# Performance work log

Measured on AMD Instinct MI355X. Metric: run time of the kernel, lower is better.

## Reference

```python
import jax, jax.numpy as jnp
import numpy as np
import math

B, CK, CV, O, T, H, W = 2, 64, 512, 2, 16, 30, 54


def setup_inputs() -> dict:
    key = jax.random.key(0)
    k1, k2, k3, k4, k5 = jax.random.split(key, 5)
    return {
        'query_key': jax.random.normal(k1, (B, CK, H, W), jnp.float32),
        'query_selection': jax.random.uniform(k2, (B, CK, H, W), jnp.float32),
        'memory_key': jax.random.normal(k3, (B, CK, T, H, W), jnp.float32),
        'memory_shrinkage': jax.random.uniform(k4, (B, 1, T, H, W), jnp.float32),
        'memory_value': jax.random.normal(k5, (B, O, CV, T, H, W), jnp.float32),
    }


def reference(query_key, query_selection, memory_key, memory_shrinkage, memory_value):
    b, ck, h, w = query_key.shape
    t = memory_key.shape[2]
    n = t * h * w          # memory bank size
    hw = h * w             # query size
    o, cv = memory_value.shape[1], memory_value.shape[2]

    mk = memory_key.reshape(b, ck, n)             # B CK N
    ms = memory_shrinkage.reshape(b, 1, n)        # B 1 N
    qk = query_key.reshape(b, ck, hw)             # B CK HW
    qe = query_selection.reshape(b, ck, hw)       # B CK HW

    # negative squared L2 distance, selection-weighted per channel:
    # -sum_c qe_c * (mk_c - qk_c)^2 = -a_sq + 2ab - b_sq
    a_sq = jnp.einsum('bcn,bcq->bnq', mk * mk, qe)          # B N HW
    two_ab = 2.0 * jnp.einsum('bcn,bcq->bnq', mk, qk * qe)  # B N HW
    b_sq = jnp.sum(qe * qk * qk, axis=1, keepdims=True)     # B 1 HW
    similarity = (-a_sq + two_ab - b_sq)
    # shrinkage scaling + 1/sqrt(CK)
    similarity = similarity * ms.reshape(b, n, 1) * (1.0 / math.sqrt(ck))

    # softmax over the memory axis N
    affinity = jax.nn.softmax(similarity, axis=1)           # B N HW

    # weighted readout
    mv = memory_value.reshape(b, o * cv, n)                 # B (O*CV) N
    mem = jnp.einsum('bvn,bnq->bvq', mv, affinity)          # B (O*CV) HW
    return mem.reshape(b, o, cv, h, w)
```

## Files before the change

### kernel.cpp

```cpp
#include <hip/hip_runtime.h>
#include <stdint.h>

#define NTOT 25920
#define OCV  1024
#define HW   1620
#define QPAD 1632
#define NBLK 810
#define KSP  8

#define MV2_STRIDE ((size_t)8 * NBLK * 4096)
#define MKP_STRIDE ((size_t)NTOT * 128)
#define QP_STRIDE  ((size_t)1664 * 128)
#define BSQ_STRIDE ((size_t)1664)
#define P_STRIDE   ((size_t)NBLK * QPAD * 32)
#define PO_STRIDE  ((size_t)KSP * OCV * QPAD)
#define LP_STRIDE  ((size_t)405 * QPAD)
#define LQ_STRIDE  ((size_t)QPAD)

typedef _Float16 f16x8 __attribute__((ext_vector_type(8)));
typedef _Float16 f16x4 __attribute__((ext_vector_type(4)));
typedef float f32x4 __attribute__((ext_vector_type(4)));

__device__ __forceinline__ void gload_lds16(const void* g, void* l) {
  __builtin_amdgcn_global_load_lds(
      (const __attribute__((address_space(1))) uint32_t*)g,
      (__attribute__((address_space(3))) uint32_t*)l, 16, 0, 0);
}

__global__ __launch_bounds__(256) void k_prep_mv2(const float* __restrict__ mv,
                                                  _Float16* __restrict__ mv2,
                                                  int bBase) {
  const int nblk = blockIdx.x, vblk = blockIdx.y, bg = blockIdx.z, t = threadIdx.x;
  const float* mvb = mv + (size_t)(bBase + bg) * OCV * NTOT;
  _Float16* outb = mv2 + (size_t)bg * MV2_STRIDE + ((size_t)(vblk * NBLK + nblk)) * 4096;
  #pragma unroll
  for (int r = 0; r < 2; ++r) {
    int idx = t + r * 256;
    int row = idx >> 2, s = idx & 3, j = s ^ ((row >> 1) & 3);
    const float* src = mvb + ((size_t)(vblk * 128 + row)) * NTOT + nblk * 32 + j * 8;
    float4 a = *((const float4*)src);
    float4 c = *((const float4*)(src + 4));
    f16x8 o;
    o[0]=(_Float16)a.x; o[1]=(_Float16)a.y; o[2]=(_Float16)a.z; o[3]=(_Float16)a.w;
    o[4]=(_Float16)c.x; o[5]=(_Float16)c.y; o[6]=(_Float16)c.z; o[7]=(_Float16)c.w;
    *((f16x8*)(outb + (size_t)idx * 8)) = o;
  }
}

__global__ __launch_bounds__(256) void k_prep_mk(const float* __restrict__ mk,
                                                 _Float16* __restrict__ mkp,
                                                 int bBase) {
  __shared__ _Float16 LT[64 * 128];
  const int bg = blockIdx.y;
  const float* mkb = mk + (size_t)(bBase + bg) * 64 * NTOT;
  _Float16* mkpb = mkp + (size_t)bg * MKP_STRIDE;
  int n0 = blockIdx.x * 64;
  int c4 = threadIdx.x >> 6, nl = threadIdx.x & 63;
  for (int c = c4; c < 64; c += 4) {
    float v = mkb[(size_t)c * NTOT + n0 + nl];
    LT[nl * 128 + c]      = (_Float16)v;
    LT[nl * 128 + 64 + c] = (_Float16)(v * v);
  }
  __syncthreads();
  #pragma unroll
  for (int k = 0; k < 4; ++k) {
    int idx = threadIdx.x + 256 * k;
    int n = idx >> 4, c16 = idx & 15;
    *((uint4*)(mkpb + ((size_t)(n0 + n)) * 128 + c16 * 8)) =
        *((const uint4*)(&LT[n * 128 + c16 * 8]));
  }
}

__global__ __launch_bounds__(128) void k_prep_q(const float* __restrict__ qk,
                                                const float* __restrict__ qe,
                                                _Float16* __restrict__ qp,
                                                float* __restrict__ bsq,
                                                int bBase) {
  __shared__ _Float16 LT[128 * 128];
  const int bg = blockIdx.y;
  const float* qkb = qk + (size_t)(bBase + bg) * 64 * HW;
  const float* qeb = qe + (size_t)(bBase + bg) * 64 * HW;
  _Float16* qpb = qp + (size_t)bg * QP_STRIDE;
  int q0 = blockIdx.x * 128;
  int t = threadIdx.x;
  int q = q0 + t;
  bool valid = q < HW;
  float acc = 0.f;
  for (int c = 0; c < 64; ++c) {
    float a = valid ? qkb[(size_t)c * HW + q] : 0.f;
    float e = valid ? qeb[(size_t)c * HW + q] : 0.f;
    LT[t * 128 + c]      = (_Float16)(2.f * a * e);
    LT[t * 128 + 64 + c] = (_Float16)(-e);
    acc += e * a * a;
  }
  bsq[(size_t)bg * BSQ_STRIDE + q] = acc;
  __syncthreads();
  #pragma unroll
  for (int k = 0; k < 16; ++k) {
    int idx = t + 128 * k;
    int qq = idx >> 4, c16 = idx & 15;
    *((uint4*)(qpb + ((size_t)(q0 + qq)) * 128 + c16 * 8)) =
        *((const uint4*)(&LT[qq * 128 + c16 * 8]));
  }
}

__global__ __launch_bounds__(256) void k_S(const _Float16* __restrict__ mkp,
                                           const _Float16* __restrict__ qp,
                                           const float* __restrict__ bsq,
                                           const float* __restrict__ ms,
                                           _Float16* __restrict__ P,
                                           float* __restrict__ lpart,
                                           int bBase) {
  const int wgid = blockIdx.x;
  const int xcd = wgid & 7;
  int kk = wgid >> 3;
  const int bg = kk / 867;
  kk -= bg * 867;
  const int nloc = kk / 17, qt = kk % 17;
  const int cntn = (xcd < 5) ? 51 : 50;
  if (nloc >= cntn) return;
  const int base = (xcd < 5) ? xcd * 51 : 255 + (xcd - 5) * 50;
  const int nunit = base + nloc;
  const int n0 = nunit * 64, q0 = qt * 96;

  const _Float16* mkpb = mkp + (size_t)bg * MKP_STRIDE;
  const _Float16* qpb  = qp + (size_t)bg * QP_STRIDE;
  const float* bsqb    = bsq + (size_t)bg * BSQ_STRIDE;
  const float* msb     = ms + (size_t)(bBase + bg) * NTOT;
  _Float16* Pb         = P + (size_t)bg * P_STRIDE;
  float* lpb           = lpart + (size_t)bg * LP_STRIDE;

  const int t = threadIdx.x;
  const int w = t >> 6, l = t & 63, l15 = l & 15, g = l >> 4;
  const int ns = w >> 1, qs = w & 1;

  f16x8 qf[3][4]; float bq[3];
  #pragma unroll
  for (int qi = 0; qi < 3; ++qi) {
    int q = q0 + qs * 48 + qi * 16 + l15;
    #pragma unroll
    for (int ks = 0; ks < 4; ++ks)
      qf[qi][ks] = *((const f16x8*)(qpb + (size_t)q * 128 + (ks * 4 + g) * 8));
    bq[qi] = bsqb[q];
  }
  f16x8 af[2][4];
  #pragma unroll
  for (int nt = 0; nt < 2; ++nt) {
    int n = n0 + ns * 32 + nt * 16 + l15;
    #pragma unroll
    for (int ks = 0; ks < 4; ++ks)
      af[nt][ks] = *((const f16x8*)(mkpb + (size_t)n * 128 + (ks * 4 + g) * 8));
  }
  f32x4 sacc[2][3];
  #pragma unroll
  for (int nt = 0; nt < 2; ++nt)
    #pragma unroll
    for (int qi = 0; qi < 3; ++qi) sacc[nt][qi] = (f32x4)0.f;
  #pragma unroll
  for (int ks = 0; ks < 4; ++ks)
    #pragma unroll
    for (int nt = 0; nt < 2; ++nt)
      #pragma unroll
      for (int qi = 0; qi < 3; ++qi)
        sacc[nt][qi] = __builtin_amdgcn_mfma_f32_16x16x32_f16(af[nt][ks], qf[qi][ks], sacc[nt][qi], 0, 0, 0);

  const float K = 0.125f * 1.44269504f;
  float4 mm[2];
  #pragma unroll
  for (int nt = 0; nt < 2; ++nt)
    mm[nt] = *((const float4*)(msb + n0 + ns * 32 + nt * 16 + g * 4));
  float psum[3] = {0.f, 0.f, 0.f};
  #pragma unroll
  for (int nt = 0; nt < 2; ++nt) {
    float m0 = mm[nt].x * K, m1 = mm[nt].y * K, m2 = mm[nt].z * K, m3 = mm[nt].w * K;
    #pragma unroll
    for (int qi = 0; qi < 3; ++qi) {
      int q = q0 + qs * 48 + qi * 16 + l15;
      float bqv = bq[qi];
      float p0 = exp2f((sacc[nt][qi][0] - bqv) * m0);
      float p1 = exp2f((sacc[nt][qi][1] - bqv) * m1);
      float p2 = exp2f((sacc[nt][qi][2] - bqv) * m2);
      float p3 = exp2f((sacc[nt][qi][3] - bqv) * m3);
      psum[qi] += (p0 + p1) + (p2 + p3);
      f16x4 ph;
      ph[0]=(_Float16)p0; ph[1]=(_Float16)p1; ph[2]=(_Float16)p2; ph[3]=(_Float16)p3;
      int nblkP = nunit * 2 + ns;
      int s_lin = nt * 2 + (g >> 1);
      int s = s_lin ^ ((q >> 1) & 3);
      *((f16x4*)(Pb + ((size_t)nblkP * QPAD + q) * 32 + s * 8 + (g & 1) * 4)) = ph;
    }
  }
  #pragma unroll
  for (int qi = 0; qi < 3; ++qi) {
    psum[qi] += __shfl_xor(psum[qi], 16);
    psum[qi] += __shfl_xor(psum[qi], 32);
  }
  __shared__ float LR[2][96];
  if (g == 0) {
    #pragma unroll
    for (int qi = 0; qi < 3; ++qi) LR[ns][qs * 48 + qi * 16 + l15] = psum[qi];
  }
  __syncthreads();
  if (t < 96) lpb[(size_t)nunit * QPAD + q0 + t] = LR[0][t] + LR[1][t];
}

__global__ __launch_bounds__(256) void k_lsum(const float* __restrict__ lpart,
                                              float* __restrict__ lout) {
  const int bg = blockIdx.y;
  int q = blockIdx.x * 256 + threadIdx.x;
  if (q >= QPAD) return;
  const float* lpb = lpart + (size_t)bg * LP_STRIDE;
  float s = 0.f;
  #pragma unroll 5
  for (int i = 0; i < 405; ++i) s += lpb[(size_t)i * QPAD + q];
  lout[(size_t)bg * LQ_STRIDE + q] = s;
}

__global__ __launch_bounds__(256) void k_RO(const _Float16* __restrict__ mv2,
                                            const _Float16* __restrict__ P,
                                            _Float16* __restrict__ pO) {
  const int wgid = blockIdx.x;
  const int ksp = wgid & 7;
  int kk = wgid >> 3;
  const int bg = kk / 136;
  kk -= bg * 136;
  const int qt = kk % 17, vblk = kk / 17;
  const int mn = (ksp < 2) ? ksp : 2;
  const int start = ksp * 101 + mn;
  const int cnt = 101 + (ksp < 2 ? 1 : 0);

  const _Float16* mv2b = mv2 + (size_t)bg * MV2_STRIDE;
  const _Float16* Pb   = P + (size_t)bg * P_STRIDE;
  _Float16* pOb        = pO + (size_t)bg * PO_STRIDE;

  const int t = threadIdx.x;
  const int w = t >> 6, l = t & 63, l15 = l & 15, g = l >> 4;
  const int wv = w >> 1, wq = w & 1;

  __shared__ _Float16 As[2][4096];
  __shared__ _Float16 Bs[2][3072];

  f32x4 acc[4][3];
  #pragma unroll
  for (int i = 0; i < 4; ++i)
    #pragma unroll
    for (int j = 0; j < 3; ++j) acc[i][j] = (f32x4)0.f;

  auto stage = [&](int nblk, int buf) {
    const char* a = (const char*)(mv2b + ((size_t)(vblk * NBLK + nblk)) * 4096);
    char* da = (char*)As[buf];
    gload_lds16(a + t * 16, da + t * 16);
    gload_lds16(a + 4096 + t * 16, da + 4096 + t * 16);
    const char* bsrc = (const char*)(Pb + ((size_t)nblk * QPAD + qt * 96) * 32);
    char* db = (char*)Bs[buf];
    gload_lds16(bsrc + t * 16, db + t * 16);
    if (t < 128) gload_lds16(bsrc + 4096 + t * 16, db + 4096 + t * 16);
  };

  stage(start, 0);
  asm volatile("s_waitcnt vmcnt(0)" ::: "memory");
  __builtin_amdgcn_s_barrier();
  __builtin_amdgcn_sched_barrier(0);

  for (int it = 0; it < cnt; ++it) {
    const int cur = it & 1, nxt = cur ^ 1;
    if (it + 1 < cnt) stage(start + it + 1, nxt);
    const _Float16* Ac = As[cur];
    const _Float16* Bc = Bs[cur];
    f16x8 av[4], bp[3];
    #pragma unroll
    for (int i = 0; i < 4; ++i) {
      int v_loc = wv * 64 + i * 16 + l15;
      av[i] = *((const f16x8*)(Ac + v_loc * 32 + ((g ^ ((v_loc >> 1) & 3)) * 8)));
    }
    #pragma unroll
    for (int j = 0; j < 3; ++j) {
      int q_loc = wq * 48 + j * 16 + l15;
      bp[j] = *((const f16x8*)(Bc + q_loc * 32 + ((g ^ ((q_loc >> 1) & 3)) * 8)));
    }
    #pragma unroll
    for (int i = 0; i < 4; ++i)
      #pragma unroll
      for (int j = 0; j < 3; ++j)
        acc[i][j] = __builtin_amdgcn_mfma_f32_16x16x32_f16(av[i], bp[j], acc[i][j], 0, 0, 0);
    asm volatile("s_waitcnt vmcnt(0) lgkmcnt(0)" ::: "memory");
    __builtin_amdgcn_s_barrier();
    __builtin_amdgcn_sched_barrier(0);
  }

  #pragma unroll
  for (int i = 0; i < 4; ++i) {
    #pragma unroll
    for (int j = 0; j < 3; ++j) {
      int qg = qt * 96 + wq * 48 + j * 16 + l15;
      #pragma unroll
      for (int r = 0; r < 4; ++r) {
        int v = vblk * 128 + wv * 64 + i * 16 + g * 4 + r;
        pOb[((size_t)ksp * OCV + v) * QPAD + qg] = (_Float16)acc[i][j][r];
      }
    }
  }
}

__global__ __launch_bounds__(256) void k_final(const _Float16* __restrict__ pO,
                                               const float* __restrict__ lq,
                                               float* __restrict__ out,
                                               int bBase) {
  int i = blockIdx.x * 256 + threadIdx.x;
  int q = i % HW;
  int rest = i / HW;
  int v = rest & (OCV - 1);
  int bg = rest >> 10;
  const _Float16* pOb = pO + (size_t)bg * PO_STRIDE;
  float s = 0.f;
  #pragma unroll
  for (int sp = 0; sp < KSP; ++sp)
    s += (float)pOb[((size_t)sp * OCV + v) * QPAD + q];
  out[((size_t)(bBase + bg) * OCV + v) * HW + q] = s / lq[(size_t)bg * LQ_STRIDE + q];
}

static void run_batch(const float* qk, const float* qe, const float* mk,
                      const float* ms, const float* mv, float* out,
                      char* ws, int bBase, int NB, hipStream_t stream) {
  char* p = ws;
  _Float16* mv2 = (_Float16*)p; p += (size_t)NB * MV2_STRIDE * 2;
  _Float16* mkp = (_Float16*)p; p += (size_t)NB * MKP_STRIDE * 2;
  _Float16* qp  = (_Float16*)p; p += (size_t)NB * QP_STRIDE * 2;
  float* bsq    = (float*)p;    p += (size_t)NB * BSQ_STRIDE * 4;
  _Float16* P   = (_Float16*)p; p += (size_t)NB * P_STRIDE * 2;
  _Float16* pO  = (_Float16*)p; p += (size_t)NB * PO_STRIDE * 2;
  float* lpart  = (float*)p;    p += (size_t)NB * LP_STRIDE * 4;
  float* lq     = (float*)p;

  k_prep_mv2<<<dim3(NBLK, 8, NB), 256, 0, stream>>>(mv, mv2, bBase);
  k_prep_mk<<<dim3(405, NB), 256, 0, stream>>>(mk, mkp, bBase);
  k_prep_q<<<dim3(13, NB), 128, 0, stream>>>(qk, qe, qp, bsq, bBase);
  k_S<<<8 * 867 * NB, 256, 0, stream>>>(mkp, qp, bsq, ms, P, lpart, bBase);
  k_lsum<<<dim3(7, NB), 256, 0, stream>>>(lpart, lq);
  k_RO<<<8 * 136 * NB, 256, 0, stream>>>(mv2, P, pO);
  k_final<<<6480 * NB, 256, 0, stream>>>(pO, lq, out, bBase);
}

extern "C" void kernel_launch(void* const* d_in, const int* in_sizes, int n_in,
                              void* d_out, int out_size, void* d_ws, size_t ws_size,
                              hipStream_t stream) {
  const float* qk = (const float*)d_in[0];
  const float* qe = (const float*)d_in[1];
  const float* mk = (const float*)d_in[2];
  const float* ms = (const float*)d_in[3];
  const float* mv = (const float*)d_in[4];
  float* out = (float*)d_out;

  const size_t per_b = MV2_STRIDE * 2 + MKP_STRIDE * 2 + QP_STRIDE * 2 + BSQ_STRIDE * 4
                     + P_STRIDE * 2 + PO_STRIDE * 2 + LP_STRIDE * 4 + LQ_STRIDE * 4;
  if (ws_size >= 2 * per_b) {
    run_batch(qk, qe, mk, ms, mv, out, (char*)d_ws, 0, 2, stream);
  } else if (ws_size >= per_b) {
    run_batch(qk, qe, mk, ms, mv, out, (char*)d_ws, 0, 1, stream);
    run_batch(qk, qe, mk, ms, mv, out, (char*)d_ws, 1, 1, stream);
  }
}
```

Baseline: 497.0 us.

## Double readout V-tile to 256 and switch to 32x32x16 MFMA

The readout GEMM kernel now gives each workgroup 256 value rows instead of 128. Each wave computes a 64x96 tile using 32x32x16 MFMA instructions in place of 16x16x32, which halves the workgroup count and lets each staged P tile be reused across twice as many value rows. It also reduces the LDS fragment loads needed per MFMA. In exchange, LDS use per block and accumulator register pressure grow, and fewer workgroups (1088) are available to fill the GPU.

```diff
diff --git a/kernel.cpp b/kernel.cpp
--- a/kernel.cpp
+++ b/kernel.cpp
@@ -20,6 +20,7 @@
 typedef _Float16 f16x8 __attribute__((ext_vector_type(8)));
 typedef _Float16 f16x4 __attribute__((ext_vector_type(4)));
 typedef float f32x4 __attribute__((ext_vector_type(4)));
+typedef float f32x16 __attribute__((ext_vector_type(16)));
 
 __device__ __forceinline__ void gload_lds16(const void* g, void* l) {
   __builtin_amdgcn_global_load_lds(
@@ -222,9 +223,9 @@
   const int wgid = blockIdx.x;
   const int ksp = wgid & 7;
   int kk = wgid >> 3;
-  const int bg = kk / 136;
-  kk -= bg * 136;
-  const int qt = kk % 17, vblk = kk / 17;
+  const int bg = kk / 68;
+  kk -= bg * 68;
+  const int qt = kk % 17, vb2 = kk / 17;
   const int mn = (ksp < 2) ? ksp : 2;
   const int start = ksp * 101 + mn;
   const int cnt = 101 + (ksp < 2 ? 1 : 0);
@@ -234,23 +235,25 @@
   _Float16* pOb        = pO + (size_t)bg * PO_STRIDE;
 
   const int t = threadIdx.x;
-  const int w = t >> 6, l = t & 63, l15 = l & 15, g = l >> 4;
-  const int wv = w >> 1, wq = w & 1;
-
-  __shared__ _Float16 As[2][4096];
+  const int w = t >> 6, l = t & 63, l31 = l & 31, kh = l >> 5;
+
+  __shared__ _Float16 As[2][8192];
   __shared__ _Float16 Bs[2][3072];
 
-  f32x4 acc[4][3];
-  #pragma unroll
-  for (int i = 0; i < 4; ++i)
-    #pragma unroll
-    for (int j = 0; j < 3; ++j) acc[i][j] = (f32x4)0.f;
+  f32x16 acc[2][3];
+  #pragma unroll
+  for (int i = 0; i < 2; ++i)
+    #pragma unroll
+    for (int j = 0; j < 3; ++j) acc[i][j] = (f32x16)0.f;
 
   auto stage = [&](int nblk, int buf) {
-    const char* a = (const char*)(mv2b + ((size_t)(vblk * NBLK + nblk)) * 4096);
     char* da = (char*)As[buf];
-    gload_lds16(a + t * 16, da + t * 16);
-    gload_lds16(a + 4096 + t * 16, da + 4096 + t * 16);
+    #pragma unroll
+    for (int h = 0; h < 2; ++h) {
+      const char* a = (const char*)(mv2b + ((size_t)((vb2 * 2 + h) * NBLK + nblk)) * 4096);
+      gload_lds16(a + t * 16, da + h * 8192 + t * 16);
+      gload_lds16(a + 4096 + t * 16, da + h * 8192 + 4096 + t * 16);
+    }
     const char* bsrc = (const char*)(Pb + ((size_t)nblk * QPAD + qt * 96) * 32);
     char* db = (char*)Bs[buf];
     gload_lds16(bsrc + t * 16, db + t * 16);
@@ -267,36 +270,42 @@
     if (it + 1 < cnt) stage(start + it + 1, nxt);
     const _Float16* Ac = As[cur];
     const _Float16* Bc = Bs[cur];
-    f16x8 av[4], bp[3];
-    #pragma unroll
-    for (int i = 0; i < 4; ++i) {
-      int v_loc = wv * 64 + i * 16 + l15;
-      av[i] = *((const f16x8*)(Ac + v_loc * 32 + ((g ^ ((v_loc >> 1) & 3)) * 8)));
+    #pragma unroll
+    for (int ks = 0; ks < 2; ++ks) {
+      f16x8 av[2], bp[3];
+      #pragma unroll
+      for (int mt = 0; mt < 2; ++mt) {
+        int row = w * 64 + mt * 32 + l31;
+        int s = (ks * 2 + kh) ^ ((row >> 1) & 3);
+        av[mt] = *((const f16x8*)(Ac + row * 32 + s * 8));
+      }
+      #pragma unroll
+      for (int j = 0; j < 3; ++j) {
+        int q = j * 32 + l31;
+        int s = (ks * 2 + kh) ^ ((q >> 1) & 3);
+        bp[j] = *((const f16x8*)(Bc + q * 32 + s * 8));
+      }
+      #pragma unroll
+      for (int mt = 0; mt < 2; ++mt)
+        #pragma unroll
+        for (int j = 0; j < 3; ++j)
+          acc[mt][j] = __builtin_amdgcn_mfma_f32_32x32x16_f16(av[mt], bp[j], acc[mt][j], 0, 0, 0);
     }
-    #pragma unroll
-    for (int j = 0; j < 3; ++j) {
-      int q_loc = wq * 48 + j * 16 + l15;
-      bp[j] = *((const f16x8*)(Bc + q_loc * 32 + ((g ^ ((q_loc >> 1) & 3)) * 8)));
-    }
-    #pragma unroll
-    for (int i = 0; i < 4; ++i)
-      #pragma unroll
-      for (int j = 0; j < 3; ++j)
-        acc[i][j] = __builtin_amdgcn_mfma_f32_16x16x32_f16(av[i], bp[j], acc[i][j], 0, 0, 0);
     asm volatile("s_waitcnt vmcnt(0) lgkmcnt(0)" ::: "memory");
     __builtin_amdgcn_s_barrier();
     __builtin_amdgcn_sched_barrier(0);
   }
 
   #pragma unroll
-  for (int i = 0; i < 4; ++i) {
+  for (int mt = 0; mt < 2; ++mt) {
     #pragma unroll
     for (int j = 0; j < 3; ++j) {
-      int qg = qt * 96 + wq * 48 + j * 16 + l15;
-      #pragma unroll
-      for (int r = 0; r < 4; ++r) {
-        int v = vblk * 128 + wv * 64 + i * 16 + g * 4 + r;
-        pOb[((size_t)ksp * OCV + v) * QPAD + qg] = (_Float16)acc[i][j][r];
+      int qg = qt * 96 + j * 32 + l31;
+      #pragma unroll
+      for (int r = 0; r < 16; ++r) {
+        int rowD = (r & 3) + 8 * (r >> 2) + 4 * kh;
+        int v = vb2 * 256 + w * 64 + mt * 32 + rowD;
+        pOb[((size_t)ksp * OCV + v) * QPAD + qg] = (_Float16)acc[mt][j][r];
       }
     }
   }
@@ -337,7 +346,7 @@
   k_prep_q<<<dim3(13, NB), 128, 0, stream>>>(qk, qe, qp, bsq, bBase);
   k_S<<<8 * 867 * NB, 256, 0, stream>>>(mkp, qp, bsq, ms, P, lpart, bBase);
   k_lsum<<<dim3(7, NB), 256, 0, stream>>>(lpart, lq);
-  k_RO<<<8 * 136 * NB, 256, 0, stream>>>(mv2, P, pO);
+  k_RO<<<8 * 68 * NB, 256, 0, stream>>>(mv2, P, pO);
   k_final<<<6480 * NB, 256, 0, stream>>>(pO, lq, out, bBase);
 }
 
```

Result: slower. 592.8 us (+19.3%).
